# Kernel tuning notes

Measured on AMD Instinct MI355X. Metric: run time of the kernel, lower is better.

The kernel has to match this reference:

```python
import jax, jax.numpy as jnp
import numpy as np

SIZE = (128, 160, 128)  # (D, H, W)
BATCH, CHANNELS = 4, 1


def setup_inputs() -> dict:
    key = jax.random.key(0)
    k1, k2 = jax.random.split(key)
    src = jax.random.normal(k1, (BATCH, CHANNELS) + SIZE, dtype=jnp.float32)
    # near-identity affine [B, 3, 4] so most sampled coords land in-volume
    eye = jnp.concatenate([jnp.eye(3, dtype=jnp.float32), jnp.zeros((3, 1), jnp.float32)], axis=1)
    affine_matrix = eye[None] + 0.05 * jax.random.normal(k2, (BATCH, 3, 4), dtype=jnp.float32)
    return {"src": src, "affine_matrix": affine_matrix}


def _mesh_matrix(D, H, W):
    # rows: dim0 (D), dim1 (H), dim2 (W), ones  -> [4, N]
    gz, gy, gx = jnp.meshgrid(jnp.arange(D), jnp.arange(H), jnp.arange(W), indexing='ij')
    N = D * H * W
    return jnp.stack([gz.reshape(N), gy.reshape(N), gx.reshape(N),
                      jnp.ones((N,), jnp.int32)], axis=0).astype(jnp.float32)


def _trilinear_border(src, ix, iy, iz):
    # src: [B, C, D, H, W]; ix/iy/iz: [B, N] unnormalized pixel coords (x->W, y->H, z->D)
    B, C, D, H, W = src.shape
    # border padding: clamp coordinate before interpolation (matches PyTorch)
    ix = jnp.clip(ix, 0.0, W - 1.0)
    iy = jnp.clip(iy, 0.0, H - 1.0)
    iz = jnp.clip(iz, 0.0, D - 1.0)
    x0f, y0f, z0f = jnp.floor(ix), jnp.floor(iy), jnp.floor(iz)
    wx = (ix - x0f)[:, None, :]  # [B,1,N]
    wy = (iy - y0f)[:, None, :]
    wz = (iz - z0f)[:, None, :]
    x0 = x0f.astype(jnp.int32); x1 = jnp.minimum(x0 + 1, W - 1)
    y0 = y0f.astype(jnp.int32); y1 = jnp.minimum(y0 + 1, H - 1)
    z0 = z0f.astype(jnp.int32); z1 = jnp.minimum(z0 + 1, D - 1)
    flat = src.reshape(B, C, D * H * W)
    N = ix.shape[-1]

    def gather(zz, yy, xx):
        idx = (zz * H + yy) * W + xx  # [B, N]
        idx = jnp.broadcast_to(idx[:, None, :], (B, C, N))
        return jnp.take_along_axis(flat, idx, axis=2)  # [B, C, N]

    c000 = gather(z0, y0, x0); c001 = gather(z0, y0, x1)
    c010 = gather(z0, y1, x0); c011 = gather(z0, y1, x1)
    c100 = gather(z1, y0, x0); c101 = gather(z1, y0, x1)
    c110 = gather(z1, y1, x0); c111 = gather(z1, y1, x1)
    c00 = c000 + (c001 - c000) * wx
    c01 = c010 + (c011 - c010) * wx
    c10 = c100 + (c101 - c100) * wx
    c11 = c110 + (c111 - c110) * wx
    c0 = c00 + (c01 - c00) * wy
    c1 = c10 + (c11 - c10) * wy
    return c0 + (c1 - c0) * wz  # [B, C, N]


def reference(src, affine_matrix):
    D, H, W = SIZE
    B, C = src.shape[:2]
    mesh = _mesh_matrix(D, H, W)  # [4, N]
    loc = jnp.einsum('bij,jn->bin', affine_matrix, mesh)  # [B, 3, N] voxel coords
    sizes = jnp.array([D, H, W], jnp.float32)
    g = 2.0 * (loc / (sizes[None, :, None] - 1.0) - 0.5)  # normalized, dims (d0,d1,d2)
    # flip to grid_sample (x, y, z) ordering, then unnormalize (align_corners=False)
    ix = ((g[:, 2] + 1.0) * W - 1.0) * 0.5
    iy = ((g[:, 1] + 1.0) * H - 1.0) * 0.5
    iz = ((g[:, 0] + 1.0) * D - 1.0) * 0.5
    out = _trilinear_border(src, ix, iy, iz)  # [B, C, N]
    return out.reshape(B, C, D, H, W)
```

## Files before the change

kernel.cpp:

```cpp
#include <hip/hip_runtime.h>

#define DD 128
#define HH 160
#define WW 128
#define BB 4
#define HW  20480
#define DHW 2621440

#define TX 32
#define TY 8
#define TZ 4
#define XT (WW / TX)
#define YT (HH / TY)
#define ZT (DD / TZ)
#define NWG (XT * YT * ZT * BB)
#define NXCD 8
#define CPX (NWG / NXCD)
#define LDSF 5120
#define MAXCH (LDSF / 4)

typedef float f2 __attribute__((ext_vector_type(2), aligned(4)));
typedef float v2 __attribute__((ext_vector_type(2)));

__global__ __launch_bounds__(256)
void st_affine_kernel(const float* __restrict__ src,
                      const float* __restrict__ aff,
                      float* __restrict__ out) {
    __shared__ float lds[LDSF];

    const int wgid = blockIdx.x;
    const int lin  = (wgid & (NXCD - 1)) * CPX + (wgid >> 3);
    const int xt = lin & 3;
    const int l2 = lin >> 2;
    const int yt = l2 % YT;
    const int l3 = l2 / YT;
    const int zt = l3 & 31;
    const int b  = l3 >> 5;
    const int x0t = xt * TX, y0t = yt * TY, z0t = zt * TZ;

    const float* A = aff + b * 12;
    const float cD = 128.f/127.f, cH = 160.f/159.f, cW = 128.f/127.f;
    const float pz0 = A[0]*cD, pz1 = A[1]*cD, pz2 = A[2]*cD,  pz3 = fmaf(A[3],  cD, -0.5f);
    const float py0 = A[4]*cH, py1 = A[5]*cH, py2 = A[6]*cH,  py3 = fmaf(A[7],  cH, -0.5f);
    const float px0 = A[8]*cW, px1 = A[9]*cW, px2 = A[10]*cW, px3 = fmaf(A[11], cW, -0.5f);

    const float hz = (TZ - 1) * 0.5f, hy = (TY - 1) * 0.5f, hx = (TX - 1) * 0.5f;
    const float ccz = (float)z0t + hz, ccy = (float)y0t + hy, ccx = (float)x0t + hx;
    const float izcn = fmaf(pz0, ccz, fmaf(pz1, ccy, fmaf(pz2, ccx, pz3)));
    const float iycn = fmaf(py0, ccz, fmaf(py1, ccy, fmaf(py2, ccx, py3)));
    const float ixcn = fmaf(px0, ccz, fmaf(px1, ccy, fmaf(px2, ccx, px3)));
    const float rz = fmaf(fabsf(pz0), hz, fmaf(fabsf(pz1), hy, fmaf(fabsf(pz2), hx, 1e-3f)));
    const float ry = fmaf(fabsf(py0), hz, fmaf(fabsf(py1), hy, fmaf(fabsf(py2), hx, 1e-3f)));
    const float rx = fmaf(fabsf(px0), hz, fmaf(fabsf(px1), hy, fmaf(fabsf(px2), hx, 1e-3f)));
    const float mnz = izcn - rz, mxz = izcn + rz;
    const float mny = iycn - ry, mxy = iycn + ry;
    const float mnx = ixcn - rx, mxx = ixcn + rx;

    const bool interior =
        (mnz > 0.02f) && (mxz < 126.98f) &&
        (mny > 0.02f) && (mxy < 158.98f) &&
        (mnx > 0.02f) && (mxx < 126.98f);

    const int xlo = max(0, (int)floorf(__builtin_amdgcn_fmed3f(mnx, 0.f, 127.f)) - 1);
    const int ylo = max(0, (int)floorf(__builtin_amdgcn_fmed3f(mny, 0.f, 159.f)) - 1);
    const int zlo = max(0, (int)floorf(__builtin_amdgcn_fmed3f(mnz, 0.f, 127.f)) - 1);
    const int xhi = min(WW - 2, (int)floorf(__builtin_amdgcn_fmed3f(mxx, 0.f, 127.f)) + 1);
    const int yhi = min(HH - 2, (int)floorf(__builtin_amdgcn_fmed3f(mxy, 0.f, 159.f)) + 1);
    const int zhi = min(DD - 2, (int)floorf(__builtin_amdgcn_fmed3f(mxz, 0.f, 127.f)) + 1);

    const int xlo4  = xlo & ~3;
    const int XE4   = xhi - xlo4 + 2;
    const int YE    = yhi - ylo + 2;
    const int ZE    = zhi - zlo + 2;
    const int pitch = (XE4 + 3) & ~3;
    const int cpr   = pitch >> 2;
    const int slice = YE * pitch;
    const int totalChunks = ZE * YE * cpr;
    const bool fits = (totalChunks <= MAXCH);

    const int tid  = threadIdx.x;
    const int lane = tid & 63;
    const int wid  = tid >> 6;

    if (fits) {
        const float rcpr = 1.f / (float)cpr, rYE = 1.f / (float)YE;
        const float cprF = (float)cpr, YEfS = (float)YE;
        const float zloF = (float)zlo, yloF = (float)ylo, xlo4F = (float)xlo4;
        const float* sb = src + b * DHW;
        const int nIt = (totalChunks + 255) >> 8;
        for (int it = 0; it < nIt; ++it) {
            const int k = (it << 8) + tid;
            float kf   = (float)k;
            float rowf = floorf(fmaf(kf, rcpr, 0.5f * rcpr));
            float xif  = fmaf(-rowf, cprF, kf);
            float zif  = floorf(fmaf(rowf, rYE, 0.5f * rYE));
            float yif  = fmaf(-zif, YEfS, rowf);
            float gf   = fmaf(zloF + zif, 20480.f,
                         fmaf(yloF + yif, 128.f,
                         fmaf(xif, 4.f, xlo4F)));
            int g = min((int)gf, DHW - 4);
            __builtin_amdgcn_global_load_lds(
                (const __attribute__((address_space(1))) void*)(sb + g),
                (__attribute__((address_space(3))) void*)(lds + (size_t)(((it << 8) + (wid << 6)) * 4)),
                16, 0, 0);
        }
    }
    __syncthreads();

    const int xp = x0t + ((lane & 15) << 1);
    const int yo = y0t + (lane >> 4) + ((wid & 1) << 2);
    const int zb = z0t + ((wid >> 1) << 1);
    const float fx0 = (float)xp, fy = (float)yo, fzb = (float)zb;

    const float izb0 = fmaf(pz0, fzb, fmaf(pz1, fy, fmaf(pz2, fx0, pz3)));
    const float iyb0 = fmaf(py0, fzb, fmaf(py1, fy, fmaf(py2, fx0, py3)));
    const float ixb0 = fmaf(px0, fzb, fmaf(px1, fy, fmaf(px2, fx0, px3)));
    const float izb1 = izb0 + pz2, iyb1 = iyb0 + py2, ixb1 = ixb0 + px2;

    const float zloF = (float)zlo, yloF = (float)ylo, xlo4F = (float)xlo4;
    const float YEf = (float)YE, pitchF = (float)pitch;
    float* dst = out + (size_t)(((b * DD + zb) * HH + yo) * WW + xp);

    auto lerpL = [&](int o, float wxs, float wys, float wzs) -> float {
        f2 v00 = *(const f2*)(lds + o);
        f2 v01 = *(const f2*)(lds + o + pitch);
        f2 v10 = *(const f2*)(lds + o + slice);
        f2 v11 = *(const f2*)(lds + o + slice + pitch);
        float c00 = fmaf(v00.y - v00.x, wxs, v00.x);
        float c01 = fmaf(v01.y - v01.x, wxs, v01.x);
        float c10 = fmaf(v10.y - v10.x, wxs, v10.x);
        float c11 = fmaf(v11.y - v11.x, wxs, v11.x);
        float c0 = fmaf(c01 - c00, wys, c00);
        float c1 = fmaf(c11 - c10, wys, c10);
        return fmaf(c1 - c0, wzs, c0);
    };
    auto lerpG = [&](float cz, float cy, float cx, float wxs, float wys, float wzs) -> float {
        int o = (int)fmaf(cz, 20480.f, fmaf(cy, 128.f, cx));
        const float* p = src + b * DHW + o;
        f2 v00 = *(const f2*)(p);
        f2 v01 = *(const f2*)(p + WW);
        f2 v10 = *(const f2*)(p + HW);
        f2 v11 = *(const f2*)(p + HW + WW);
        float c00 = fmaf(v00.y - v00.x, wxs, v00.x);
        float c01 = fmaf(v01.y - v01.x, wxs, v01.x);
        float c10 = fmaf(v10.y - v10.x, wxs, v10.x);
        float c11 = fmaf(v11.y - v11.x, wxs, v11.x);
        float c0 = fmaf(c01 - c00, wys, c00);
        float c1 = fmaf(c11 - c10, wys, c10);
        return fmaf(c1 - c0, wzs, c0);
    };

#pragma unroll
    for (int kq = 0; kq < 2; ++kq) {
        const float kf = (float)kq;
        float iz0 = fmaf(kf, pz0, izb0), iz1 = fmaf(kf, pz0, izb1);
        float iy0 = fmaf(kf, py0, iyb0), iy1 = fmaf(kf, py0, iyb1);
        float ix0 = fmaf(kf, px0, ixb0), ix1 = fmaf(kf, px0, ixb1);
        float cz0, cy0, cx0, cz1, cy1, cx1;
        if (interior) {
            cz0 = floorf(iz0); cz1 = floorf(iz1);
            cy0 = floorf(iy0); cy1 = floorf(iy1);
            cx0 = floorf(ix0); cx1 = floorf(ix1);
        } else {
            iz0 = __builtin_amdgcn_fmed3f(iz0, 0.f, 127.f);
            iz1 = __builtin_amdgcn_fmed3f(iz1, 0.f, 127.f);
            iy0 = __builtin_amdgcn_fmed3f(iy0, 0.f, 159.f);
            iy1 = __builtin_amdgcn_fmed3f(iy1, 0.f, 159.f);
            ix0 = __builtin_amdgcn_fmed3f(ix0, 0.f, 127.f);
            ix1 = __builtin_amdgcn_fmed3f(ix1, 0.f, 127.f);
            cz0 = fminf(floorf(iz0), 126.f); cz1 = fminf(floorf(iz1), 126.f);
            cy0 = fminf(floorf(iy0), 158.f); cy1 = fminf(floorf(iy1), 158.f);
            cx0 = fminf(floorf(ix0), 126.f); cx1 = fminf(floorf(ix1), 126.f);
        }
        const float wz0 = iz0 - cz0, wz1 = iz1 - cz1;
        const float wy0 = iy0 - cy0, wy1 = iy1 - cy1;
        const float wx0 = ix0 - cx0, wx1 = ix1 - cx1;

        v2 r;
        if (fits) {
            int o0 = (int)fmaf(fmaf(cz0 - zloF, YEf, cy0 - yloF), pitchF, cx0 - xlo4F);
            int o1 = (int)fmaf(fmaf(cz1 - zloF, YEf, cy1 - yloF), pitchF, cx1 - xlo4F);
            r.x = lerpL(o0, wx0, wy0, wz0);
            r.y = lerpL(o1, wx1, wy1, wz1);
        } else {
            r.x = lerpG(cz0, cy0, cx0, wx0, wy0, wz0);
            r.y = lerpG(cz1, cy1, cx1, wx1, wy1, wz1);
        }
        __builtin_nontemporal_store(r, (v2*)(dst + kq * HW));
    }
}

extern "C" void kernel_launch(void* const* d_in, const int* in_sizes, int n_in,
                              void* d_out, int out_size, void* d_ws, size_t ws_size,
                              hipStream_t stream) {
    const float* src = (const float*)d_in[0];
    const float* aff = (const float*)d_in[1];
    float* out = (float*)d_out;

    st_affine_kernel<<<dim3(NWG), dim3(256), 0, stream>>>(src, aff, out);
}
```

Baseline: 28.33 us.

## Double-buffer LDS staging across z-tiles in persistent per-block loop

Each workgroup now processes eight consecutive 2-deep z tiles instead of one 4-deep tile. It stages the source bounding box for the next tile into a second LDS buffer with global_load_lds while computing the current tile, using explicit vmcnt waits and barriers. This hides global load latency behind interpolation and cuts the grid to 2560 blocks, at the cost of more LDS per block, longer serial work per block, and hand-tuned waitcnt counts that must match the fixed five staging loads.

Result: slower. 44.83 us (+58.2%).

```diff
diff --git a/kernel.cpp b/kernel.cpp
--- a/kernel.cpp
+++ b/kernel.cpp
@@ -9,24 +9,32 @@
 
 #define TX 32
 #define TY 8
-#define TZ 4
-#define XT (WW / TX)
-#define YT (HH / TY)
-#define ZT (DD / TZ)
-#define NWG (XT * YT * ZT * BB)
+#define TZ 2
+#define NT 8
+#define XT 4
+#define YT 20
+#define ZGD 8
+#define NWG 2560
 #define NXCD 8
-#define CPX (NWG / NXCD)
-#define LDSF 5120
-#define MAXCH (LDSF / 4)
+#define CPX 320
+#define NST 5
+#define BUFCH 1280
+#define BUFF 5120
 
 typedef float f2 __attribute__((ext_vector_type(2), aligned(4)));
 typedef float v2 __attribute__((ext_vector_type(2)));
 
-__global__ __launch_bounds__(256)
+struct Box {
+    float xlo4F, yloF, zloF, YEf, pitchF, cprF, rcpr, rYE;
+    int   pitchI, sliceI, nCh;
+    bool  interior;
+};
+
+__global__ __launch_bounds__(256, 4)
 void st_affine_kernel(const float* __restrict__ src,
                       const float* __restrict__ aff,
                       float* __restrict__ out) {
-    __shared__ float lds[LDSF];
+    __shared__ float lds[2 * BUFF];
 
     const int wgid = blockIdx.x;
     const int lin  = (wgid & (NXCD - 1)) * CPX + (wgid >> 3);
@@ -34,9 +42,9 @@
     const int l2 = lin >> 2;
     const int yt = l2 % YT;
     const int l3 = l2 / YT;
-    const int zt = l3 & 31;
-    const int b  = l3 >> 5;
-    const int x0t = xt * TX, y0t = yt * TY, z0t = zt * TZ;
+    const int zg = l3 & (ZGD - 1);
+    const int b  = l3 >> 3;
+    const int x0t = xt * TX, y0t = yt * TY, zbase = zg * (TZ * NT);
 
     const float* A = aff + b * 12;
     const float cD = 128.f/127.f, cH = 160.f/159.f, cW = 128.f/127.f;
@@ -45,119 +53,97 @@
     const float px0 = A[8]*cW, px1 = A[9]*cW, px2 = A[10]*cW, px3 = fmaf(A[11], cW, -0.5f);
 
     const float hz = (TZ - 1) * 0.5f, hy = (TY - 1) * 0.5f, hx = (TX - 1) * 0.5f;
-    const float ccz = (float)z0t + hz, ccy = (float)y0t + hy, ccx = (float)x0t + hx;
-    const float izcn = fmaf(pz0, ccz, fmaf(pz1, ccy, fmaf(pz2, ccx, pz3)));
-    const float iycn = fmaf(py0, ccz, fmaf(py1, ccy, fmaf(py2, ccx, py3)));
-    const float ixcn = fmaf(px0, ccz, fmaf(px1, ccy, fmaf(px2, ccx, px3)));
-    const float rz = fmaf(fabsf(pz0), hz, fmaf(fabsf(pz1), hy, fmaf(fabsf(pz2), hx, 1e-3f)));
-    const float ry = fmaf(fabsf(py0), hz, fmaf(fabsf(py1), hy, fmaf(fabsf(py2), hx, 1e-3f)));
-    const float rx = fmaf(fabsf(px0), hz, fmaf(fabsf(px1), hy, fmaf(fabsf(px2), hx, 1e-3f)));
-    const float mnz = izcn - rz, mxz = izcn + rz;
-    const float mny = iycn - ry, mxy = iycn + ry;
-    const float mnx = ixcn - rx, mxx = ixcn + rx;
-
-    const bool interior =
-        (mnz > 0.02f) && (mxz < 126.98f) &&
-        (mny > 0.02f) && (mxy < 158.98f) &&
-        (mnx > 0.02f) && (mxx < 126.98f);
-
-    const int xlo = max(0, (int)floorf(__builtin_amdgcn_fmed3f(mnx, 0.f, 127.f)) - 1);
-    const int ylo = max(0, (int)floorf(__builtin_amdgcn_fmed3f(mny, 0.f, 159.f)) - 1);
-    const int zlo = max(0, (int)floorf(__builtin_amdgcn_fmed3f(mnz, 0.f, 127.f)) - 1);
-    const int xhi = min(WW - 2, (int)floorf(__builtin_amdgcn_fmed3f(mxx, 0.f, 127.f)) + 1);
-    const int yhi = min(HH - 2, (int)floorf(__builtin_amdgcn_fmed3f(mxy, 0.f, 159.f)) + 1);
-    const int zhi = min(DD - 2, (int)floorf(__builtin_amdgcn_fmed3f(mxz, 0.f, 127.f)) + 1);
-
-    const int xlo4  = xlo & ~3;
-    const int XE4   = xhi - xlo4 + 2;
-    const int YE    = yhi - ylo + 2;
-    const int ZE    = zhi - zlo + 2;
-    const int pitch = (XE4 + 3) & ~3;
-    const int cpr   = pitch >> 2;
-    const int slice = YE * pitch;
-    const int totalChunks = ZE * YE * cpr;
-    const bool fits = (totalChunks <= MAXCH);
+    const float ccz = (float)zbase + hz, ccy = (float)y0t + hy, ccx = (float)x0t + hx;
+    const float izcn0 = fmaf(pz0, ccz, fmaf(pz1, ccy, fmaf(pz2, ccx, pz3)));
+    const float iycn0 = fmaf(py0, ccz, fmaf(py1, ccy, fmaf(py2, ccx, py3)));
+    const float ixcn0 = fmaf(px0, ccz, fmaf(px1, ccy, fmaf(px2, ccx, px3)));
+    const float rz_ = fmaf(fabsf(pz0), hz, fmaf(fabsf(pz1), hy, fmaf(fabsf(pz2), hx, 1e-3f)));
+    const float ry_ = fmaf(fabsf(py0), hz, fmaf(fabsf(py1), hy, fmaf(fabsf(py2), hx, 1e-3f)));
+    const float rx_ = fmaf(fabsf(px0), hz, fmaf(fabsf(px1), hy, fmaf(fabsf(px2), hx, 1e-3f)));
+    const float dz2 = 2.f * pz0, dy2 = 2.f * py0, dx2 = 2.f * px0;
+
+    auto makeBox = [&](float izc, float iyc, float ixc) -> Box {
+        Box B;
+        float mnz = izc - rz_, mxz = izc + rz_;
+        float mny = iyc - ry_, mxy = iyc + ry_;
+        float mnx = ixc - rx_, mxx = ixc + rx_;
+        B.interior = (mnz > 0.02f) && (mxz < 126.98f) &&
+                     (mny > 0.02f) && (mxy < 158.98f) &&
+                     (mnx > 0.02f) && (mxx < 126.98f);
+        int xlo = max(0, (int)floorf(__builtin_amdgcn_fmed3f(mnx, 0.f, 127.f)) - 1);
+        int ylo = max(0, (int)floorf(__builtin_amdgcn_fmed3f(mny, 0.f, 159.f)) - 1);
+        int zlo = max(0, (int)floorf(__builtin_amdgcn_fmed3f(mnz, 0.f, 127.f)) - 1);
+        int xhi = min(WW - 2, (int)floorf(__builtin_amdgcn_fmed3f(mxx, 0.f, 127.f)) + 1);
+        int yhi = min(HH - 2, (int)floorf(__builtin_amdgcn_fmed3f(mxy, 0.f, 159.f)) + 1);
+        int zhi = min(DD - 2, (int)floorf(__builtin_amdgcn_fmed3f(mxz, 0.f, 127.f)) + 1);
+        int xlo4 = xlo & ~3;
+        int XE4  = xhi - xlo4 + 2;
+        int pitch = (XE4 + 3) & ~3;
+        int cpr   = pitch >> 2;
+        int YE = yhi - ylo + 2, ZE = zhi - zlo + 2;
+        B.pitchI = pitch; B.sliceI = YE * pitch;
+        B.nCh = ZE * YE * cpr;
+        B.xlo4F = (float)xlo4; B.yloF = (float)ylo; B.zloF = (float)zlo;
+        B.YEf = (float)YE; B.pitchF = (float)pitch; B.cprF = (float)cpr;
+        B.rcpr = 1.f / (float)cpr; B.rYE = 1.f / (float)YE;
+        return B;
+    };
+
+    bool allfit = true;
+    {
+        float a = izcn0, c2 = iycn0, c3 = ixcn0;
+#pragma unroll 1
+        for (int t = 0; t < NT; ++t) {
+            Box bx = makeBox(a, c2, c3);
+            allfit = allfit && (bx.nCh <= BUFCH);
+            a += dz2; c2 += dy2; c3 += dx2;
+        }
+    }
 
     const int tid  = threadIdx.x;
     const int lane = tid & 63;
     const int wid  = tid >> 6;
 
-    if (fits) {
-        const float rcpr = 1.f / (float)cpr, rYE = 1.f / (float)YE;
-        const float cprF = (float)cpr, YEfS = (float)YE;
-        const float zloF = (float)zlo, yloF = (float)ylo, xlo4F = (float)xlo4;
-        const float* sb = src + b * DHW;
-        const int nIt = (totalChunks + 255) >> 8;
-        for (int it = 0; it < nIt; ++it) {
-            const int k = (it << 8) + tid;
-            float kf   = (float)k;
-            float rowf = floorf(fmaf(kf, rcpr, 0.5f * rcpr));
-            float xif  = fmaf(-rowf, cprF, kf);
-            float zif  = floorf(fmaf(rowf, rYE, 0.5f * rYE));
-            float yif  = fmaf(-zif, YEfS, rowf);
-            float gf   = fmaf(zloF + zif, 20480.f,
-                         fmaf(yloF + yif, 128.f,
-                         fmaf(xif, 4.f, xlo4F)));
+    const int xp  = x0t + ((lane & 15) << 1);
+    const int yo  = y0t + (lane >> 4) + ((wid & 1) << 2);
+    const int zin = wid >> 1;
+
+    const float fx0 = (float)xp, fy = (float)yo, fzb = (float)(zbase + zin);
+    const float izb00 = fmaf(pz0, fzb, fmaf(pz1, fy, fmaf(pz2, fx0, pz3)));
+    const float iyb00 = fmaf(py0, fzb, fmaf(py1, fy, fmaf(py2, fx0, py3)));
+    const float ixb00 = fmaf(px0, fzb, fmaf(px1, fy, fmaf(px2, fx0, px3)));
+
+    const float* sb = src + b * DHW;
+    float* dst0 = out + (size_t)(((b * DD + zbase + zin) * HH + yo) * WW + xp);
+
+    auto stage = [&](int bufIdx, const Box& B) {
+        float* bbuf = lds + bufIdx * BUFF;
+#pragma unroll
+        for (int it = 0; it < NST; ++it) {
+            int k = (it << 8) + tid;
+            float kf   = (float)min(k, B.nCh - 1);
+            float rowf = floorf(fmaf(kf, B.rcpr, 0.5f * B.rcpr));
+            float xif  = fmaf(-rowf, B.cprF, kf);
+            float zif  = floorf(fmaf(rowf, B.rYE, 0.5f * B.rYE));
+            float yif  = fmaf(-zif, B.YEf, rowf);
+            float gf   = fmaf(B.zloF + zif, 20480.f,
+                         fmaf(B.yloF + yif, 128.f,
+                         fmaf(xif, 4.f, B.xlo4F)));
             int g = min((int)gf, DHW - 4);
             __builtin_amdgcn_global_load_lds(
                 (const __attribute__((address_space(1))) void*)(sb + g),
-                (__attribute__((address_space(3))) void*)(lds + (size_t)(((it << 8) + (wid << 6)) * 4)),
+                (__attribute__((address_space(3))) void*)(bbuf + (((it << 8) + (wid << 6)) << 2)),
                 16, 0, 0);
         }
-    }
-    __syncthreads();
-
-    const int xp = x0t + ((lane & 15) << 1);
-    const int yo = y0t + (lane >> 4) + ((wid & 1) << 2);
-    const int zb = z0t + ((wid >> 1) << 1);
-    const float fx0 = (float)xp, fy = (float)yo, fzb = (float)zb;
-
-    const float izb0 = fmaf(pz0, fzb, fmaf(pz1, fy, fmaf(pz2, fx0, pz3)));
-    const float iyb0 = fmaf(py0, fzb, fmaf(py1, fy, fmaf(py2, fx0, py3)));
-    const float ixb0 = fmaf(px0, fzb, fmaf(px1, fy, fmaf(px2, fx0, px3)));
-    const float izb1 = izb0 + pz2, iyb1 = iyb0 + py2, ixb1 = ixb0 + px2;
-
-    const float zloF = (float)zlo, yloF = (float)ylo, xlo4F = (float)xlo4;
-    const float YEf = (float)YE, pitchF = (float)pitch;
-    float* dst = out + (size_t)(((b * DD + zb) * HH + yo) * WW + xp);
-
-    auto lerpL = [&](int o, float wxs, float wys, float wzs) -> float {
-        f2 v00 = *(const f2*)(lds + o);
-        f2 v01 = *(const f2*)(lds + o + pitch);
-        f2 v10 = *(const f2*)(lds + o + slice);
-        f2 v11 = *(const f2*)(lds + o + slice + pitch);
-        float c00 = fmaf(v00.y - v00.x, wxs, v00.x);
-        float c01 = fmaf(v01.y - v01.x, wxs, v01.x);
-        float c10 = fmaf(v10.y - v10.x, wxs, v10.x);
-        float c11 = fmaf(v11.y - v11.x, wxs, v11.x);
-        float c0 = fmaf(c01 - c00, wys, c00);
-        float c1 = fmaf(c11 - c10, wys, c10);
-        return fmaf(c1 - c0, wzs, c0);
     };
-    auto lerpG = [&](float cz, float cy, float cx, float wxs, float wys, float wzs) -> float {
-        int o = (int)fmaf(cz, 20480.f, fmaf(cy, 128.f, cx));
-        const float* p = src + b * DHW + o;
-        f2 v00 = *(const f2*)(p);
-        f2 v01 = *(const f2*)(p + WW);
-        f2 v10 = *(const f2*)(p + HW);
-        f2 v11 = *(const f2*)(p + HW + WW);
-        float c00 = fmaf(v00.y - v00.x, wxs, v00.x);
-        float c01 = fmaf(v01.y - v01.x, wxs, v01.x);
-        float c10 = fmaf(v10.y - v10.x, wxs, v10.x);
-        float c11 = fmaf(v11.y - v11.x, wxs, v11.x);
-        float c0 = fmaf(c01 - c00, wys, c00);
-        float c1 = fmaf(c11 - c10, wys, c10);
-        return fmaf(c1 - c0, wzs, c0);
-    };
-
-#pragma unroll
-    for (int kq = 0; kq < 2; ++kq) {
-        const float kf = (float)kq;
-        float iz0 = fmaf(kf, pz0, izb0), iz1 = fmaf(kf, pz0, izb1);
-        float iy0 = fmaf(kf, py0, iyb0), iy1 = fmaf(kf, py0, iyb1);
-        float ix0 = fmaf(kf, px0, ixb0), ix1 = fmaf(kf, px0, ixb1);
+
+    auto computeTile = [&](const Box& B, int bufIdx, float tf2, float* dstT) {
+        const float* bbuf = lds + bufIdx * BUFF;
+        float iz0 = fmaf(tf2, pz0, izb00), iz1 = iz0 + pz2;
+        float iy0 = fmaf(tf2, py0, iyb00), iy1 = iy0 + py2;
+        float ix0 = fmaf(tf2, px0, ixb00), ix1 = ix0 + px2;
         float cz0, cy0, cx0, cz1, cy1, cx1;
-        if (interior) {
+        if (B.interior) {
             cz0 = floorf(iz0); cz1 = floorf(iz1);
             cy0 = floorf(iy0); cy1 = floorf(iy1);
             cx0 = floorf(ix0); cx1 = floorf(ix1);
@@ -172,21 +158,110 @@
             cy0 = fminf(floorf(iy0), 158.f); cy1 = fminf(floorf(iy1), 158.f);
             cx0 = fminf(floorf(ix0), 126.f); cx1 = fminf(floorf(ix1), 126.f);
         }
-        const float wz0 = iz0 - cz0, wz1 = iz1 - cz1;
-        const float wy0 = iy0 - cy0, wy1 = iy1 - cy1;
-        const float wx0 = ix0 - cx0, wx1 = ix1 - cx1;
-
+        float wz0 = iz0 - cz0, wz1 = iz1 - cz1;
+        float wy0 = iy0 - cy0, wy1 = iy1 - cy1;
+        float wx0 = ix0 - cx0, wx1 = ix1 - cx1;
+        int o0 = (int)fmaf(fmaf(cz0 - B.zloF, B.YEf, cy0 - B.yloF), B.pitchF, cx0 - B.xlo4F);
+        int o1 = (int)fmaf(fmaf(cz1 - B.zloF, B.YEf, cy1 - B.yloF), B.pitchF, cx1 - B.xlo4F);
+        const int pi = B.pitchI, sl = B.sliceI;
         v2 r;
-        if (fits) {
-            int o0 = (int)fmaf(fmaf(cz0 - zloF, YEf, cy0 - yloF), pitchF, cx0 - xlo4F);
-            int o1 = (int)fmaf(fmaf(cz1 - zloF, YEf, cy1 - yloF), pitchF, cx1 - xlo4F);
-            r.x = lerpL(o0, wx0, wy0, wz0);
-            r.y = lerpL(o1, wx1, wy1, wz1);
-        } else {
-            r.x = lerpG(cz0, cy0, cx0, wx0, wy0, wz0);
-            r.y = lerpG(cz1, cy1, cx1, wx1, wy1, wz1);
-        }
-        __builtin_nontemporal_store(r, (v2*)(dst + kq * HW));
+        {
+            f2 v00 = *(const f2*)(bbuf + o0);
+            f2 v01 = *(const f2*)(bbuf + o0 + pi);
+            f2 v10 = *(const f2*)(bbuf + o0 + sl);
+            f2 v11 = *(const f2*)(bbuf + o0 + sl + pi);
+            float c00 = fmaf(v00.y - v00.x, wx0, v00.x);
+            float c01 = fmaf(v01.y - v01.x, wx0, v01.x);
+            float c10 = fmaf(v10.y - v10.x, wx0, v10.x);
+            float c11 = fmaf(v11.y - v11.x, wx0, v11.x);
+            float c0 = fmaf(c01 - c00, wy0, c00);
+            float c1 = fmaf(c11 - c10, wy0, c10);
+            r.x = fmaf(c1 - c0, wz0, c0);
+        }
+        {
+            f2 v00 = *(const f2*)(bbuf + o1);
+            f2 v01 = *(const f2*)(bbuf + o1 + pi);
+            f2 v10 = *(const f2*)(bbuf + o1 + sl);
+            f2 v11 = *(const f2*)(bbuf + o1 + sl + pi);
+            float c00 = fmaf(v00.y - v00.x, wx1, v00.x);
+            float c01 = fmaf(v01.y - v01.x, wx1, v01.x);
+            float c10 = fmaf(v10.y - v10.x, wx1, v10.x);
+            float c11 = fmaf(v11.y - v11.x, wx1, v11.x);
+            float c0 = fmaf(c01 - c00, wy1, c00);
+            float c1 = fmaf(c11 - c10, wy1, c10);
+            r.y = fmaf(c1 - c0, wz1, c0);
+        }
+        __builtin_nontemporal_store(r, (v2*)dstT);
+    };
+
+    if (allfit) {
+        Box Bc = makeBox(izcn0, iycn0, ixcn0);
+        stage(0, Bc);
+        float czc = izcn0 + dz2, cyc = iycn0 + dy2, cxc = ixcn0 + dx2;
+        Box Bn = makeBox(czc, cyc, cxc);
+        stage(1, Bn);
+        asm volatile("s_waitcnt vmcnt(5)" ::: "memory");
+        __builtin_amdgcn_s_barrier();
+        computeTile(Bc, 0, 0.f, dst0);
+        asm volatile("s_waitcnt lgkmcnt(0)" ::: "memory");
+        __builtin_amdgcn_sched_barrier(0);
+        __builtin_amdgcn_s_barrier();
+        Bc = Bn;
+#pragma unroll 1
+        for (int t = 1; t < NT - 1; ++t) {
+            czc += dz2; cyc += dy2; cxc += dx2;
+            Bn = makeBox(czc, cyc, cxc);
+            stage((t + 1) & 1, Bn);
+            asm volatile("s_waitcnt vmcnt(6)" ::: "memory");
+            __builtin_amdgcn_s_barrier();
+            computeTile(Bc, t & 1, 2.f * (float)t, dst0 + t * (2 * HW));
+            asm volatile("s_waitcnt lgkmcnt(0)" ::: "memory");
+            __builtin_amdgcn_sched_barrier(0);
+            __builtin_amdgcn_s_barrier();
+            Bc = Bn;
+        }
+        asm volatile("s_waitcnt vmcnt(1)" ::: "memory");
+        __builtin_amdgcn_s_barrier();
+        computeTile(Bc, (NT - 1) & 1, 2.f * (float)(NT - 1), dst0 + (NT - 1) * (2 * HW));
+    } else {
+#pragma unroll 1
+        for (int t = 0; t < NT; ++t) {
+            float tf2 = 2.f * (float)t;
+            float iz0 = fmaf(tf2, pz0, izb00), iz1 = iz0 + pz2;
+            float iy0 = fmaf(tf2, py0, iyb00), iy1 = iy0 + py2;
+            float ix0 = fmaf(tf2, px0, ixb00), ix1 = ix0 + px2;
+            iz0 = __builtin_amdgcn_fmed3f(iz0, 0.f, 127.f);
+            iz1 = __builtin_amdgcn_fmed3f(iz1, 0.f, 127.f);
+            iy0 = __builtin_amdgcn_fmed3f(iy0, 0.f, 159.f);
+            iy1 = __builtin_amdgcn_fmed3f(iy1, 0.f, 159.f);
+            ix0 = __builtin_amdgcn_fmed3f(ix0, 0.f, 127.f);
+            ix1 = __builtin_amdgcn_fmed3f(ix1, 0.f, 127.f);
+            float cz0 = fminf(floorf(iz0), 126.f), cz1 = fminf(floorf(iz1), 126.f);
+            float cy0 = fminf(floorf(iy0), 158.f), cy1 = fminf(floorf(iy1), 158.f);
+            float cx0 = fminf(floorf(ix0), 126.f), cx1 = fminf(floorf(ix1), 126.f);
+            float wz0 = iz0 - cz0, wz1 = iz1 - cz1;
+            float wy0 = iy0 - cy0, wy1 = iy1 - cy1;
+            float wx0 = ix0 - cx0, wx1 = ix1 - cx1;
+            auto g1 = [&](float cz, float cy, float cx, float wxs, float wys, float wzs) -> float {
+                int o = (int)fmaf(cz, 20480.f, fmaf(cy, 128.f, cx));
+                const float* p = sb + o;
+                f2 v00 = *(const f2*)(p);
+                f2 v01 = *(const f2*)(p + WW);
+                f2 v10 = *(const f2*)(p + HW);
+                f2 v11 = *(const f2*)(p + HW + WW);
+                float c00 = fmaf(v00.y - v00.x, wxs, v00.x);
+                float c01 = fmaf(v01.y - v01.x, wxs, v01.x);
+                float c10 = fmaf(v10.y - v10.x, wxs, v10.x);
+                float c11 = fmaf(v11.y - v11.x, wxs, v11.x);
+                float c0 = fmaf(c01 - c00, wys, c00);
+                float c1 = fmaf(c11 - c10, wys, c10);
+                return fmaf(c1 - c0, wzs, c0);
+            };
+            v2 r;
+            r.x = g1(cz0, cy0, cx0, wx0, wy0, wz0);
+            r.y = g1(cz1, cy1, cx1, wx1, wy1, wz1);
+            __builtin_nontemporal_store(r, (v2*)(dst0 + t * (2 * HW)));
+        }
     }
 }
 
```

## Double z-depth of workgroup tiles and specialize interior/border sampling loops

Applied to the files above, without the earlier changes.

Each workgroup now covers 8 z-slices instead of 4, with every thread producing 4 z-steps of 2 outputs. The LDS staging buffer grows to hold the larger source footprint, which amortizes halo loads and per-workgroup setup over more outputs. The sampling loops are split into separate interior LDS, border LDS and global-fallback paths, and coordinates are advanced incrementally. This halves the grid, which may reduce occupancy or load balance, and the larger footprint may more often fail to fit and fall back to global reads.

Result: faster. 24.66 us (-13.0%).

```diff
diff --git a/kernel.cpp b/kernel.cpp
--- a/kernel.cpp
+++ b/kernel.cpp
@@ -9,14 +9,14 @@
 
 #define TX 32
 #define TY 8
-#define TZ 4
-#define XT (WW / TX)
-#define YT (HH / TY)
-#define ZT (DD / TZ)
+#define TZ 8
+#define XT 4
+#define YT 20
+#define ZT 16
 #define NWG (XT * YT * ZT * BB)
 #define NXCD 8
 #define CPX (NWG / NXCD)
-#define LDSF 5120
+#define LDSF 7168
 #define MAXCH (LDSF / 4)
 
 typedef float f2 __attribute__((ext_vector_type(2), aligned(4)));
@@ -34,8 +34,8 @@
     const int l2 = lin >> 2;
     const int yt = l2 % YT;
     const int l3 = l2 / YT;
-    const int zt = l3 & 31;
-    const int b  = l3 >> 5;
+    const int zt = l3 & (ZT - 1);
+    const int b  = l3 >> 4;
     const int x0t = xt * TX, y0t = yt * TY, z0t = zt * TZ;
 
     const float* A = aff + b * 12;
@@ -82,11 +82,24 @@
     const int lane = tid & 63;
     const int wid  = tid >> 6;
 
+    const float zloF = (float)zlo, yloF = (float)ylo, xlo4F = (float)xlo4;
+    const float YEf = (float)YE, pitchF = (float)pitch;
+
+    const int xp = x0t + ((lane & 15) << 1);
+    const int yo = y0t + (lane >> 4) + ((wid & 1) << 2);
+    const int zb = z0t + ((wid >> 1) << 2);
+    const float fx0 = (float)xp, fy = (float)yo, fzb = (float)zb;
+
+    const float izb0 = fmaf(pz0, fzb, fmaf(pz1, fy, fmaf(pz2, fx0, pz3)));
+    const float iyb0 = fmaf(py0, fzb, fmaf(py1, fy, fmaf(py2, fx0, py3)));
+    const float ixb0 = fmaf(px0, fzb, fmaf(px1, fy, fmaf(px2, fx0, px3)));
+
+    const float* sb = src + b * DHW;
+    float* dst0 = out + (size_t)(((b * DD + zb) * HH + yo) * WW + xp);
+
     if (fits) {
         const float rcpr = 1.f / (float)cpr, rYE = 1.f / (float)YE;
-        const float cprF = (float)cpr, YEfS = (float)YE;
-        const float zloF = (float)zlo, yloF = (float)ylo, xlo4F = (float)xlo4;
-        const float* sb = src + b * DHW;
+        const float cprF = (float)cpr;
         const int nIt = (totalChunks + 255) >> 8;
         for (int it = 0; it < nIt; ++it) {
             const int k = (it << 8) + tid;
@@ -94,7 +107,7 @@
             float rowf = floorf(fmaf(kf, rcpr, 0.5f * rcpr));
             float xif  = fmaf(-rowf, cprF, kf);
             float zif  = floorf(fmaf(rowf, rYE, 0.5f * rYE));
-            float yif  = fmaf(-zif, YEfS, rowf);
+            float yif  = fmaf(-zif, YEf, rowf);
             float gf   = fmaf(zloF + zif, 20480.f,
                          fmaf(yloF + yif, 128.f,
                          fmaf(xif, 4.f, xlo4F)));
@@ -104,89 +117,109 @@
                 (__attribute__((address_space(3))) void*)(lds + (size_t)(((it << 8) + (wid << 6)) * 4)),
                 16, 0, 0);
         }
-    }
-    __syncthreads();
-
-    const int xp = x0t + ((lane & 15) << 1);
-    const int yo = y0t + (lane >> 4) + ((wid & 1) << 2);
-    const int zb = z0t + ((wid >> 1) << 1);
-    const float fx0 = (float)xp, fy = (float)yo, fzb = (float)zb;
-
-    const float izb0 = fmaf(pz0, fzb, fmaf(pz1, fy, fmaf(pz2, fx0, pz3)));
-    const float iyb0 = fmaf(py0, fzb, fmaf(py1, fy, fmaf(py2, fx0, py3)));
-    const float ixb0 = fmaf(px0, fzb, fmaf(px1, fy, fmaf(px2, fx0, px3)));
-    const float izb1 = izb0 + pz2, iyb1 = iyb0 + py2, ixb1 = ixb0 + px2;
-
-    const float zloF = (float)zlo, yloF = (float)ylo, xlo4F = (float)xlo4;
-    const float YEf = (float)YE, pitchF = (float)pitch;
-    float* dst = out + (size_t)(((b * DD + zb) * HH + yo) * WW + xp);
-
-    auto lerpL = [&](int o, float wxs, float wys, float wzs) -> float {
-        f2 v00 = *(const f2*)(lds + o);
-        f2 v01 = *(const f2*)(lds + o + pitch);
-        f2 v10 = *(const f2*)(lds + o + slice);
-        f2 v11 = *(const f2*)(lds + o + slice + pitch);
-        float c00 = fmaf(v00.y - v00.x, wxs, v00.x);
-        float c01 = fmaf(v01.y - v01.x, wxs, v01.x);
-        float c10 = fmaf(v10.y - v10.x, wxs, v10.x);
-        float c11 = fmaf(v11.y - v11.x, wxs, v11.x);
-        float c0 = fmaf(c01 - c00, wys, c00);
-        float c1 = fmaf(c11 - c10, wys, c10);
-        return fmaf(c1 - c0, wzs, c0);
-    };
-    auto lerpG = [&](float cz, float cy, float cx, float wxs, float wys, float wzs) -> float {
-        int o = (int)fmaf(cz, 20480.f, fmaf(cy, 128.f, cx));
-        const float* p = src + b * DHW + o;
-        f2 v00 = *(const f2*)(p);
-        f2 v01 = *(const f2*)(p + WW);
-        f2 v10 = *(const f2*)(p + HW);
-        f2 v11 = *(const f2*)(p + HW + WW);
-        float c00 = fmaf(v00.y - v00.x, wxs, v00.x);
-        float c01 = fmaf(v01.y - v01.x, wxs, v01.x);
-        float c10 = fmaf(v10.y - v10.x, wxs, v10.x);
-        float c11 = fmaf(v11.y - v11.x, wxs, v11.x);
-        float c0 = fmaf(c01 - c00, wys, c00);
-        float c1 = fmaf(c11 - c10, wys, c10);
-        return fmaf(c1 - c0, wzs, c0);
-    };
-
+        __syncthreads();
+
+        auto lerpL = [&](int o, float wxs, float wys, float wzs) -> float {
+            f2 v00 = *(const f2*)(lds + o);
+            f2 v01 = *(const f2*)(lds + o + pitch);
+            f2 v10 = *(const f2*)(lds + o + slice);
+            f2 v11 = *(const f2*)(lds + o + slice + pitch);
+            float c00 = fmaf(v00.y - v00.x, wxs, v00.x);
+            float c01 = fmaf(v01.y - v01.x, wxs, v01.x);
+            float c10 = fmaf(v10.y - v10.x, wxs, v10.x);
+            float c11 = fmaf(v11.y - v11.x, wxs, v11.x);
+            float c0 = fmaf(c01 - c00, wys, c00);
+            float c1 = fmaf(c11 - c10, wys, c10);
+            return fmaf(c1 - c0, wzs, c0);
+        };
+
+        if (interior) {
+            float az0 = izb0 - zloF, ay0 = iyb0 - yloF, ax0 = ixb0 - xlo4F;
+            float az1 = az0 + pz2,   ay1 = ay0 + py2,   ax1 = ax0 + px2;
 #pragma unroll
-    for (int kq = 0; kq < 2; ++kq) {
-        const float kf = (float)kq;
-        float iz0 = fmaf(kf, pz0, izb0), iz1 = fmaf(kf, pz0, izb1);
-        float iy0 = fmaf(kf, py0, iyb0), iy1 = fmaf(kf, py0, iyb1);
-        float ix0 = fmaf(kf, px0, ixb0), ix1 = fmaf(kf, px0, ixb1);
-        float cz0, cy0, cx0, cz1, cy1, cx1;
-        if (interior) {
-            cz0 = floorf(iz0); cz1 = floorf(iz1);
-            cy0 = floorf(iy0); cy1 = floorf(iy1);
-            cx0 = floorf(ix0); cx1 = floorf(ix1);
+            for (int s = 0; s < 4; ++s) {
+                float cz0 = floorf(az0), cz1 = floorf(az1);
+                float cy0 = floorf(ay0), cy1 = floorf(ay1);
+                float cx0 = floorf(ax0), cx1 = floorf(ax1);
+                float wz0 = az0 - cz0, wz1 = az1 - cz1;
+                float wy0 = ay0 - cy0, wy1 = ay1 - cy1;
+                float wx0 = ax0 - cx0, wx1 = ax1 - cx1;
+                int o0 = (int)fmaf(fmaf(cz0, YEf, cy0), pitchF, cx0);
+                int o1 = (int)fmaf(fmaf(cz1, YEf, cy1), pitchF, cx1);
+                v2 r;
+                r.x = lerpL(o0, wx0, wy0, wz0);
+                r.y = lerpL(o1, wx1, wy1, wz1);
+                __builtin_nontemporal_store(r, (v2*)(dst0 + s * HW));
+                az0 += pz0; ay0 += py0; ax0 += px0;
+                az1 += pz0; ay1 += py0; ax1 += px0;
+            }
         } else {
-            iz0 = __builtin_amdgcn_fmed3f(iz0, 0.f, 127.f);
-            iz1 = __builtin_amdgcn_fmed3f(iz1, 0.f, 127.f);
-            iy0 = __builtin_amdgcn_fmed3f(iy0, 0.f, 159.f);
-            iy1 = __builtin_amdgcn_fmed3f(iy1, 0.f, 159.f);
-            ix0 = __builtin_amdgcn_fmed3f(ix0, 0.f, 127.f);
-            ix1 = __builtin_amdgcn_fmed3f(ix1, 0.f, 127.f);
-            cz0 = fminf(floorf(iz0), 126.f); cz1 = fminf(floorf(iz1), 126.f);
-            cy0 = fminf(floorf(iy0), 158.f); cy1 = fminf(floorf(iy1), 158.f);
-            cx0 = fminf(floorf(ix0), 126.f); cx1 = fminf(floorf(ix1), 126.f);
+            float az0 = izb0, ay0 = iyb0, ax0 = ixb0;
+            float az1 = az0 + pz2, ay1 = ay0 + py2, ax1 = ax0 + px2;
+#pragma unroll
+            for (int s = 0; s < 4; ++s) {
+                float iz0 = __builtin_amdgcn_fmed3f(az0, 0.f, 127.f);
+                float iz1 = __builtin_amdgcn_fmed3f(az1, 0.f, 127.f);
+                float iy0 = __builtin_amdgcn_fmed3f(ay0, 0.f, 159.f);
+                float iy1 = __builtin_amdgcn_fmed3f(ay1, 0.f, 159.f);
+                float ix0 = __builtin_amdgcn_fmed3f(ax0, 0.f, 127.f);
+                float ix1 = __builtin_amdgcn_fmed3f(ax1, 0.f, 127.f);
+                float cz0 = fminf(floorf(iz0), 126.f), cz1 = fminf(floorf(iz1), 126.f);
+                float cy0 = fminf(floorf(iy0), 158.f), cy1 = fminf(floorf(iy1), 158.f);
+                float cx0 = fminf(floorf(ix0), 126.f), cx1 = fminf(floorf(ix1), 126.f);
+                float wz0 = iz0 - cz0, wz1 = iz1 - cz1;
+                float wy0 = iy0 - cy0, wy1 = iy1 - cy1;
+                float wx0 = ix0 - cx0, wx1 = ix1 - cx1;
+                int o0 = (int)fmaf(fmaf(cz0 - zloF, YEf, cy0 - yloF), pitchF, cx0 - xlo4F);
+                int o1 = (int)fmaf(fmaf(cz1 - zloF, YEf, cy1 - yloF), pitchF, cx1 - xlo4F);
+                v2 r;
+                r.x = lerpL(o0, wx0, wy0, wz0);
+                r.y = lerpL(o1, wx1, wy1, wz1);
+                __builtin_nontemporal_store(r, (v2*)(dst0 + s * HW));
+                az0 += pz0; ay0 += py0; ax0 += px0;
+                az1 += pz0; ay1 += py0; ax1 += px0;
+            }
         }
-        const float wz0 = iz0 - cz0, wz1 = iz1 - cz1;
-        const float wy0 = iy0 - cy0, wy1 = iy1 - cy1;
-        const float wx0 = ix0 - cx0, wx1 = ix1 - cx1;
-
-        v2 r;
-        if (fits) {
-            int o0 = (int)fmaf(fmaf(cz0 - zloF, YEf, cy0 - yloF), pitchF, cx0 - xlo4F);
-            int o1 = (int)fmaf(fmaf(cz1 - zloF, YEf, cy1 - yloF), pitchF, cx1 - xlo4F);
-            r.x = lerpL(o0, wx0, wy0, wz0);
-            r.y = lerpL(o1, wx1, wy1, wz1);
-        } else {
-            r.x = lerpG(cz0, cy0, cx0, wx0, wy0, wz0);
-            r.y = lerpG(cz1, cy1, cx1, wx1, wy1, wz1);
+    } else {
+        __syncthreads();
+        float az0 = izb0, ay0 = iyb0, ax0 = ixb0;
+        float az1 = az0 + pz2, ay1 = ay0 + py2, ax1 = ax0 + px2;
+#pragma unroll
+        for (int s = 0; s < 4; ++s) {
+            float iz0 = __builtin_amdgcn_fmed3f(az0, 0.f, 127.f);
+            float iz1 = __builtin_amdgcn_fmed3f(az1, 0.f, 127.f);
+            float iy0 = __builtin_amdgcn_fmed3f(ay0, 0.f, 159.f);
+            float iy1 = __builtin_amdgcn_fmed3f(ay1, 0.f, 159.f);
+            float ix0 = __builtin_amdgcn_fmed3f(ax0, 0.f, 127.f);
+            float ix1 = __builtin_amdgcn_fmed3f(ax1, 0.f, 127.f);
+            float cz0 = fminf(floorf(iz0), 126.f), cz1 = fminf(floorf(iz1), 126.f);
+            float cy0 = fminf(floorf(iy0), 158.f), cy1 = fminf(floorf(iy1), 158.f);
+            float cx0 = fminf(floorf(ix0), 126.f), cx1 = fminf(floorf(ix1), 126.f);
+            float wz0 = iz0 - cz0, wz1 = iz1 - cz1;
+            float wy0 = iy0 - cy0, wy1 = iy1 - cy1;
+            float wx0 = ix0 - cx0, wx1 = ix1 - cx1;
+            auto g1 = [&](float cz, float cy, float cx, float wxs, float wys, float wzs) -> float {
+                int o = (int)fmaf(cz, 20480.f, fmaf(cy, 128.f, cx));
+                const float* p = sb + o;
+                f2 v00 = *(const f2*)(p);
+                f2 v01 = *(const f2*)(p + WW);
+                f2 v10 = *(const f2*)(p + HW);
+                f2 v11 = *(const f2*)(p + HW + WW);
+                float c00 = fmaf(v00.y - v00.x, wxs, v00.x);
+                float c01 = fmaf(v01.y - v01.x, wxs, v01.x);
+                float c10 = fmaf(v10.y - v10.x, wxs, v10.x);
+                float c11 = fmaf(v11.y - v11.x, wxs, v11.x);
+                float c0 = fmaf(c01 - c00, wys, c00);
+                float c1 = fmaf(c11 - c10, wys, c10);
+                return fmaf(c1 - c0, wzs, c0);
+            };
+            v2 r;
+            r.x = g1(cz0, cy0, cx0, wx0, wy0, wz0);
+            r.y = g1(cz1, cy1, cx1, wx1, wy1, wz1);
+            __builtin_nontemporal_store(r, (v2*)(dst0 + s * HW));
+            az0 += pz0; ay0 += py0; ax0 += px0;
+            az1 += pz0; ay1 += py0; ax1 += px0;
         }
-        __builtin_nontemporal_store(r, (v2*)(dst + kq * HW));
     }
 }
 
```
